# Kernel tuning notes

Hardware: AMD Instinct MI355X
Metric: run time of the kernel (lower is better)

The kernel has to match this reference:

```python
import jax, jax.numpy as jnp
import numpy as np

A = 9  # len(scales) * len(ratios) anchor templates
DN = ('NHWC', 'HWIO', 'NHWC')


def _conv(x, w, b):
    y = jax.lax.conv_general_dilated(x, w, window_strides=(1, 1), padding='SAME',
                                     dimension_numbers=DN)
    return y + b


def setup_inputs() -> dict:
    key = jax.random.key(0)
    ks = jax.random.split(key, 9)
    s = 0.02  # weight init scale
    x = jax.random.normal(ks[0], (4, 128, 128, 512), jnp.float32)
    W1 = jax.random.normal(ks[1], (3, 3, 512, 256), jnp.float32) * s
    b1 = jnp.zeros((256,), jnp.float32)
    W2 = jax.random.normal(ks[2], (3, 3, 256, 256), jnp.float32) * s
    b2 = jnp.zeros((256,), jnp.float32)
    Wr = jax.random.normal(ks[3], (1, 1, 256, 4 * A), jnp.float32) * s
    br = jnp.zeros((4 * A,), jnp.float32)
    Wc = jax.random.normal(ks[4], (1, 1, 256, 2 * A), jnp.float32) * s
    bc = jnp.zeros((2 * A,), jnp.float32)
    return {'x': x, 'W1': W1, 'b1': b1, 'W2': W2, 'b2': b2,
            'Wr': Wr, 'br': br, 'Wc': Wc, 'bc': bc}


def reference(x, W1, b1, W2, b2, Wr, br, Wc, bc):
    h = jax.nn.relu(_conv(x, W1, b1))
    h = jax.nn.relu(_conv(h, W2, b2))
    B, H, W = h.shape[0], h.shape[1], h.shape[2]
    reg = _conv(h, Wr, br).reshape(B, H, W, A, 4)            # (B,H,W,A,4)
    cls = _conv(h, Wc, bc).reshape(B, H, W, A, 2)            # (B,H,W,A,2)
    cls = jax.nn.softmax(cls, axis=4)
    return jnp.concatenate((cls, reg), axis=4)               # (B,H,W,A,6)
```

## Files before the change

### kernel.cpp

```cpp
#include <hip/hip_runtime.h>


typedef float f32x4  __attribute__((ext_vector_type(4)));
typedef float f32x16 __attribute__((ext_vector_type(16)));
typedef short bf16x8 __attribute__((ext_vector_type(8)));

union U16x8 { uint4 v; unsigned short s[8]; };

__device__ __forceinline__ unsigned short f2bf(float f) {
  union { float f; unsigned int u; } v; v.f = f;
  unsigned int r = v.u + 0x7FFFu + ((v.u >> 16) & 1u);
  return (unsigned short)(r >> 16);
}

#define GLOAD_LDS16(G, L)                                        \
  __builtin_amdgcn_global_load_lds(                              \
      (const __attribute__((address_space(1))) void*)(G),        \
      (__attribute__((address_space(3))) void*)(L), 16, 0, 0)

__global__ __launch_bounds__(256) void transpose_cvt(
    const float* __restrict__ src, unsigned short* __restrict__ dst,
    int K, int N) {
  __shared__ float t[32][33];
  const int tx = threadIdx.x, ty = threadIdx.y;
  const int k0 = blockIdx.x * 32, n0 = blockIdx.y * 32;
  const float* s = src + (size_t)blockIdx.z * K * N;
  unsigned short* d = dst + (size_t)blockIdx.z * N * K;
#pragma unroll
  for (int r = 0; r < 32; r += 8) {
    int k = k0 + ty + r, n = n0 + tx;
    t[ty + r][tx] = (k < K && n < N) ? s[(size_t)k * N + n] : 0.f;
  }
  __syncthreads();
#pragma unroll
  for (int r = 0; r < 32; r += 8) {
    int n = n0 + ty + r, k = k0 + tx;
    if (n < N && k < K) d[(size_t)n * K + k] = f2bf(t[tx][ty + r]);
  }
}

__global__ __launch_bounds__(256) void convert_x(
    const float* __restrict__ x, unsigned short* __restrict__ xp) {
  int idx = blockIdx.x * 256 + threadIdx.x;
  int g = idx & 63;
  int cell = idx >> 6;
  int xpix = cell % 130;
  int t = cell / 130;
  int ypix = t % 130;
  int b = t / 130;
  U16x8 u;
  if (xpix == 0 || xpix == 129 || ypix == 0 || ypix == 129) {
    u.v = make_uint4(0u, 0u, 0u, 0u);
  } else {
    const float* sp = x + ((size_t)((b * 128 + ypix - 1) * 128) + (xpix - 1)) * 512 + g * 8;
    float4 a = *(const float4*)sp;
    float4 c = *(const float4*)(sp + 4);
    u.s[0] = f2bf(a.x); u.s[1] = f2bf(a.y); u.s[2] = f2bf(a.z); u.s[3] = f2bf(a.w);
    u.s[4] = f2bf(c.x); u.s[5] = f2bf(c.y); u.s[6] = f2bf(c.z); u.s[7] = f2bf(c.w);
  }
  *(uint4*)(xp + (size_t)cell * 512 + g * 8) = u.v;
}

__global__ __launch_bounds__(256) void zero_h1_borders(unsigned short* __restrict__ h1p) {
  int idx = blockIdx.x * 256 + threadIdx.x;
  int g = idx & 31;
  int cell = idx >> 5;
  int xpix = cell % 130;
  int t = cell / 130;
  int ypix = t % 130;
  if (xpix == 0 || xpix == 129 || ypix == 0 || ypix == 129)
    *(uint4*)(h1p + (size_t)cell * 256 + g * 8) = make_uint4(0u, 0u, 0u, 0u);
}

template<int CIN, int MODE>
__global__ __launch_bounds__(512, 2) void conv3x3(
    const unsigned short* __restrict__ Ap,
    const unsigned short* __restrict__ WT,
    const float* __restrict__ bias,
    unsigned short* __restrict__ out) {
  constexpr int NCI    = CIN / 32;
  constexpr int LOGNCI = (NCI == 16) ? 4 : 3;
  constexpr int NT     = 3 * NCI;
  constexpr int A_BYTES = 8 * 192 * 16;
  constexpr int B_BYTES = 12 * 256 * 16;
  constexpr int BUF     = A_BYTES + B_BYTES;
  __shared__ __align__(16) unsigned char smem[2 * BUF];

  const int tid  = threadIdx.x;
  const int wave = tid >> 6, lane = tid & 63;
  const int l31 = lane & 31, hi = lane >> 5;
  const int wm = wave >> 2, wn = wave & 3;
  const int b = blockIdx.x >> 6;
  const int y0 = (blockIdx.x & 63) * 2;
  const int brow = b * 130 + y0;

  int a_go[3], a_ld[3];
#pragma unroll
  for (int i = 0; i < 3; ++i) {
    int c = (wave * 3 + i) * 64 + lane;
    int px = c % 192, t = c / 192;
    int q = t & 3, rw = t >> 2;
    a_go[i] = (rw * 130 + px) * CIN + q * 8;
    a_ld[i] = (wave * 3 + i) * 1024;
  }
  int b_go[6], b_ld[6];
#pragma unroll
  for (int i = 0; i < 6; ++i) {
    int c = (wave * 6 + i) * 64 + lane;
    int co = c & 255, t = c >> 8;
    int q = t & 3, dxs = t >> 2;
    b_go[i] = (dxs * 256 + co) * CIN + q * 8;
    b_ld[i] = A_BYTES + (wave * 6 + i) * 1024;
  }

  const float bb0 = bias[wn * 64 + l31];
  const float bb1 = bias[wn * 64 + 32 + l31];

  f32x16 acc[4][2] = {};

  auto stage = [&](int tile) {
    const int dy  = tile >> LOGNCI;
    const int ci0 = (tile & (NCI - 1)) << 5;
    unsigned char* sb = smem + (size_t)(tile & 1) * BUF;
    const unsigned short* Ab = Ap + (size_t)(brow + dy) * 130 * CIN + ci0;
#pragma unroll
    for (int i = 0; i < 3; ++i)
      GLOAD_LDS16(Ab + a_go[i], sb + a_ld[i]);
    const unsigned short* Bb = WT + (size_t)dy * 3 * 256 * CIN + ci0;
#pragma unroll
    for (int i = 0; i < 6; ++i)
      GLOAD_LDS16(Bb + b_go[i], sb + b_ld[i]);
  };

  stage(0);
  asm volatile("s_waitcnt vmcnt(0)" ::: "memory");
  __builtin_amdgcn_s_barrier();

#pragma unroll 2
  for (int t = 0; t < NT; ++t) {
    const unsigned char* sb = smem + (size_t)(t & 1) * BUF;
#pragma unroll
    for (int dx = 0; dx < 3; ++dx) {
      bf16x8 af[2][4], bfr[2][2];
#pragma unroll
      for (int ks = 0; ks < 2; ++ks) {
        const int q_ = ks * 2 + hi;
        const int ab = ((wm * 4 + q_) * 192 + dx + l31) * 16;
        const int bb = A_BYTES + ((dx * 4 + q_) * 256 + wn * 64 + l31) * 16;
#pragma unroll
        for (int i = 0; i < 4; ++i)
          af[ks][i] = *(const bf16x8*)(sb + ab + i * 512);
#pragma unroll
        for (int j = 0; j < 2; ++j)
          bfr[ks][j] = *(const bf16x8*)(sb + bb + j * 512);
      }
      if (dx == 0 && t + 1 < NT) stage(t + 1);
      if (dx == 2 && t + 1 < NT)
        asm volatile("s_waitcnt vmcnt(0)" ::: "memory");
      __builtin_amdgcn_sched_barrier(0);
      __builtin_amdgcn_s_barrier();
      asm volatile("s_waitcnt lgkmcnt(0)" ::: "memory");
      __builtin_amdgcn_sched_barrier(0);
      __builtin_amdgcn_s_setprio(1);
#pragma unroll
      for (int ks = 0; ks < 2; ++ks)
#pragma unroll
        for (int i = 0; i < 4; ++i)
#pragma unroll
          for (int j = 0; j < 2; ++j)
            acc[i][j] = __builtin_amdgcn_mfma_f32_32x32x16_bf16(
                af[ks][i], bfr[ks][j], acc[i][j], 0, 0, 0);
      __builtin_amdgcn_s_setprio(0);
      __builtin_amdgcn_sched_barrier(0);
      __builtin_amdgcn_s_barrier();
    }
  }

#pragma unroll
  for (int i = 0; i < 4; ++i) {
#pragma unroll
    for (int j = 0; j < 2; ++j) {
      const int n = wn * 64 + j * 32 + l31;
      const float bb = j ? bb1 : bb0;
#pragma unroll
      for (int reg = 0; reg < 16; ++reg) {
        int px = i * 32 + (reg & 3) + 8 * (reg >> 2) + 4 * hi;
        float v = fmaxf(acc[i][j][reg] + bb, 0.f);
        size_t off;
        if (MODE == 0)
          off = ((size_t)(brow + wm + 1) * 130 + (px + 1)) * 256 + n;
        else
          off = ((size_t)((b * 128 + y0 + wm) * 128) + px) * 256 + n;
        out[off] = f2bf(v);
      }
    }
  }
}

__global__ __launch_bounds__(256) void heads_kernel(
    const unsigned short* __restrict__ h2,
    const unsigned short* __restrict__ WhT,
    const float* __restrict__ br, const float* __restrict__ bc,
    float* __restrict__ out) {
  __shared__ __align__(16) unsigned short As[64][264];
  const int tid = threadIdx.x;
  const int wave = tid >> 6, lane = tid & 63;
  const int quad = lane >> 4, l16 = lane & 15;
  const int pix0 = blockIdx.x * 64;
#pragma unroll
  for (int r = 0; r < 8; ++r) {
    int s = r * 256 + tid;
    int row = s >> 5, seg = s & 31;
    *(uint4*)&As[row][seg * 8] =
        *(const uint4*)(h2 + (size_t)(pix0 + row) * 256 + seg * 8);
  }
  __syncthreads();
  f32x4 acc[4] = {};
#pragma unroll
  for (int ks = 0; ks < 8; ++ks) {
    bf16x8 af = *(const bf16x8*)&As[wave * 16 + l16][ks * 32 + quad * 8];
#pragma unroll
    for (int j = 0; j < 4; ++j) {
      bf16x8 bfr = *(const bf16x8*)(WhT + (size_t)(j * 16 + l16) * 256 + ks * 32 + quad * 8);
      acc[j] = __builtin_amdgcn_mfma_f32_16x16x32_bf16(af, bfr, acc[j], 0, 0, 0);
    }
  }
#pragma unroll
  for (int j = 0; j < 4; ++j) {
    int n = j * 16 + l16;
    float bias = 0.f;
    if (n < 18) bias = bc[n];
    else if (n < 54) bias = br[n - 18];
#pragma unroll
    for (int r = 0; r < 4; ++r) {
      int p = pix0 + wave * 16 + quad * 4 + r;
      float v = acc[j][r] + bias;
      float partner = __shfl_xor(v, 1);
      if (n < 18) {
        float mx = fmaxf(v, partner);
        float e0 = __expf(v - mx), e1 = __expf(partner - mx);
        int a = n >> 1, sl = n & 1;
        out[(size_t)p * 54 + a * 6 + sl] = e0 / (e0 + e1);
      } else if (n < 54) {
        int rr = n - 18, a = rr >> 2, sl = (rr & 3) + 2;
        out[(size_t)p * 54 + a * 6 + sl] = v;
      }
    }
  }
}

extern "C" void kernel_launch(void* const* d_in, const int* in_sizes, int n_in,
                              void* d_out, int out_size, void* d_ws, size_t ws_size,
                              hipStream_t stream) {
  const float* x  = (const float*)d_in[0];
  const float* W1 = (const float*)d_in[1];
  const float* b1 = (const float*)d_in[2];
  const float* W2 = (const float*)d_in[3];
  const float* b2 = (const float*)d_in[4];
  const float* Wr = (const float*)d_in[5];
  const float* br = (const float*)d_in[6];
  const float* Wc = (const float*)d_in[7];
  const float* bc = (const float*)d_in[8];
  float* out = (float*)d_out;

  constexpr size_t XPAD_B  = 4ull * 130 * 130 * 512 * 2;
  constexpr size_t H1PAD_B = 4ull * 130 * 130 * 256 * 2;
  constexpr size_t H2_B    = 4ull * 128 * 128 * 256 * 2;
  constexpr size_t W1T_B   = 9ull * 256 * 512 * 2;
  constexpr size_t W2T_B   = 9ull * 256 * 256 * 2;
  char* ws = (char*)d_ws;
  unsigned short* x_pad  = (unsigned short*)(ws);
  unsigned short* h1_pad = (unsigned short*)(ws + XPAD_B);
  unsigned short* h2     = (unsigned short*)(ws + XPAD_B + H1PAD_B);
  unsigned short* W1T    = (unsigned short*)(ws + XPAD_B + H1PAD_B + H2_B);
  unsigned short* W2T    = (unsigned short*)(ws + XPAD_B + H1PAD_B + H2_B + W1T_B);
  unsigned short* WhT    = (unsigned short*)(ws + XPAD_B + H1PAD_B + H2_B + W1T_B + W2T_B);

  hipMemsetAsync(WhT, 0, 64ull * 256 * 2, stream);
  transpose_cvt<<<dim3(16, 8, 9), dim3(32, 8), 0, stream>>>(W1, W1T, 512, 256);
  transpose_cvt<<<dim3(8, 8, 9),  dim3(32, 8), 0, stream>>>(W2, W2T, 256, 256);
  transpose_cvt<<<dim3(8, 1, 1),  dim3(32, 8), 0, stream>>>(Wc, WhT, 256, 18);
  transpose_cvt<<<dim3(8, 2, 1),  dim3(32, 8), 0, stream>>>(Wr, WhT + 18 * 256, 256, 36);
  convert_x<<<16900, 256, 0, stream>>>(x, x_pad);
  zero_h1_borders<<<8450, 256, 0, stream>>>(h1_pad);
  conv3x3<512, 0><<<256, 512, 0, stream>>>(x_pad, W1T, b1, h1_pad);
  conv3x3<256, 1><<<256, 512, 0, stream>>>(h1_pad, W2T, b2, h2);
  heads_kernel<<<1024, 256, 0, stream>>>(h2, WhT, br, bc, out);
}
```

Measured before the change: 551.9 us.

## Store activations channel-group-major and pre-pack weights per tile for contiguous LDS loads

```diff
diff --git a/kernel.cpp b/kernel.cpp
--- a/kernel.cpp
+++ b/kernel.cpp
@@ -37,6 +37,26 @@
     int n = n0 + ty + r, k = k0 + tx;
     if (n < N && k < K) d[(size_t)n * K + k] = f2bf(t[tx][ty + r]);
   }
+}
+
+__global__ __launch_bounds__(256) void pack_w(
+    const float* __restrict__ W, unsigned short* __restrict__ out, int CIN) {
+  const int NCI = CIN / 32;
+  int tid = blockIdx.x * 256 + threadIdx.x;
+  int co = tid & 255;
+  int q  = (tid >> 8) & 3;
+  int t  = tid >> 10;
+  int dx = t % 3;
+  int r  = t / 3;
+  int kt = r % NCI;
+  int dy = r / NCI;
+  U16x8 u;
+#pragma unroll
+  for (int e = 0; e < 8; ++e) {
+    int ci = kt * 32 + q * 8 + e;
+    u.s[e] = f2bf(W[((size_t)(dy * 3 + dx) * CIN + ci) * 256 + co]);
+  }
+  *(uint4*)(out + (size_t)tid * 8) = u.v;
 }
 
 __global__ __launch_bounds__(256) void convert_x(
@@ -58,30 +78,34 @@
     u.s[0] = f2bf(a.x); u.s[1] = f2bf(a.y); u.s[2] = f2bf(a.z); u.s[3] = f2bf(a.w);
     u.s[4] = f2bf(c.x); u.s[5] = f2bf(c.y); u.s[6] = f2bf(c.z); u.s[7] = f2bf(c.w);
   }
-  *(uint4*)(xp + (size_t)cell * 512 + g * 8) = u.v;
+  *(uint4*)(xp + (((size_t)(b * 130 + ypix) * 64 + g) * 130 + xpix) * 8) = u.v;
 }
 
 __global__ __launch_bounds__(256) void zero_h1_borders(unsigned short* __restrict__ h1p) {
   int idx = blockIdx.x * 256 + threadIdx.x;
-  int g = idx & 31;
-  int cell = idx >> 5;
-  int xpix = cell % 130;
-  int t = cell / 130;
-  int ypix = t % 130;
-  if (xpix == 0 || xpix == 129 || ypix == 0 || ypix == 129)
-    *(uint4*)(h1p + (size_t)cell * 256 + g * 8) = make_uint4(0u, 0u, 0u, 0u);
+  int px = idx % 130;
+  int t = idx / 130;
+  int g = t & 31;
+  int tt = t >> 5;
+  int y = tt % 130;
+  int b = tt / 130;
+  if (px == 0 || px == 129 || y == 0 || y == 129)
+    *(uint4*)(h1p + (((size_t)(b * 130 + y) * 32 + g) * 130 + px) * 8) =
+        make_uint4(0u, 0u, 0u, 0u);
 }
 
 template<int CIN, int MODE>
 __global__ __launch_bounds__(512, 2) void conv3x3(
     const unsigned short* __restrict__ Ap,
-    const unsigned short* __restrict__ WT,
+    const unsigned short* __restrict__ WTp,
     const float* __restrict__ bias,
     unsigned short* __restrict__ out) {
   constexpr int NCI    = CIN / 32;
   constexpr int LOGNCI = (NCI == 16) ? 4 : 3;
   constexpr int NT     = 3 * NCI;
-  constexpr int A_BYTES = 8 * 192 * 16;
+  constexpr int GPR    = CIN / 8;
+  constexpr int PXS    = 136;
+  constexpr int A_BYTES = 8 * PXS * 16;
   constexpr int B_BYTES = 12 * 256 * 16;
   constexpr int BUF     = A_BYTES + B_BYTES;
   __shared__ __align__(16) unsigned char smem[2 * BUF];
@@ -94,23 +118,17 @@
   const int y0 = (blockIdx.x & 63) * 2;
   const int brow = b * 130 + y0;
 
-  int a_go[3], a_ld[3];
+  int a_rel[3], a_c[3];
 #pragma unroll
   for (int i = 0; i < 3; ++i) {
-    int c = (wave * 3 + i) * 64 + lane;
-    int px = c % 192, t = c / 192;
-    int q = t & 3, rw = t >> 2;
-    a_go[i] = (rw * 130 + px) * CIN + q * 8;
-    a_ld[i] = (wave * 3 + i) * 1024;
-  }
-  int b_go[6], b_ld[6];
-#pragma unroll
-  for (int i = 0; i < 6; ++i) {
-    int c = (wave * 6 + i) * 64 + lane;
-    int co = c & 255, t = c >> 8;
-    int q = t & 3, dxs = t >> 2;
-    b_go[i] = (dxs * 256 + co) * CIN + q * 8;
-    b_ld[i] = A_BYTES + (wave * 6 + i) * 1024;
+    int s = wave + i * 8;
+    if (s < 17) {
+      int c = s * 64 + lane;
+      int px = c % PXS, t2 = c / PXS;
+      int q = t2 & 3, rw = t2 >> 2;
+      a_rel[i] = (rw * GPR + q) * 1040 + px * 8;
+      a_c[i] = c * 16;
+    } else { a_rel[i] = 0; a_c[i] = 0; }
   }
 
   const float bb0 = bias[wn * 64 + l31];
@@ -119,17 +137,19 @@
   f32x16 acc[4][2] = {};
 
   auto stage = [&](int tile) {
-    const int dy  = tile >> LOGNCI;
-    const int ci0 = (tile & (NCI - 1)) << 5;
+    const int dy = tile >> LOGNCI;
+    const int kt = tile & (NCI - 1);
     unsigned char* sb = smem + (size_t)(tile & 1) * BUF;
-    const unsigned short* Ab = Ap + (size_t)(brow + dy) * 130 * CIN + ci0;
-#pragma unroll
-    for (int i = 0; i < 3; ++i)
-      GLOAD_LDS16(Ab + a_go[i], sb + a_ld[i]);
-    const unsigned short* Bb = WT + (size_t)dy * 3 * 256 * CIN + ci0;
-#pragma unroll
-    for (int i = 0; i < 6; ++i)
-      GLOAD_LDS16(Bb + b_go[i], sb + b_ld[i]);
+    const unsigned short* Ab = Ap + ((size_t)(brow + dy) * GPR + kt * 4) * 1040;
+    GLOAD_LDS16(Ab + a_rel[0], sb + a_c[0]);
+    GLOAD_LDS16(Ab + a_rel[1], sb + a_c[1]);
+    if (wave == 0) GLOAD_LDS16(Ab + a_rel[2], sb + a_c[2]);
+    const unsigned short* Bb = WTp + (size_t)(dy * NCI + kt) * 24576;
+#pragma unroll
+    for (int i = 0; i < 6; ++i) {
+      int c = (wave * 6 + i) * 64 + lane;
+      GLOAD_LDS16(Bb + (size_t)c * 8, sb + A_BYTES + c * 16);
+    }
   };
 
   stage(0);
@@ -145,7 +165,7 @@
 #pragma unroll
       for (int ks = 0; ks < 2; ++ks) {
         const int q_ = ks * 2 + hi;
-        const int ab = ((wm * 4 + q_) * 192 + dx + l31) * 16;
+        const int ab = ((wm * 4 + q_) * PXS + dx + l31) * 16;
         const int bb = A_BYTES + ((dx * 4 + q_) * 256 + wn * 64 + l31) * 16;
 #pragma unroll
         for (int i = 0; i < 4; ++i)
@@ -188,7 +208,7 @@
         float v = fmaxf(acc[i][j][reg] + bb, 0.f);
         size_t off;
         if (MODE == 0)
-          off = ((size_t)(brow + wm + 1) * 130 + (px + 1)) * 256 + n;
+          off = (((size_t)(brow + wm + 1) * 32 + (n >> 3)) * 130 + (px + 1)) * 8 + (n & 7);
         else
           off = ((size_t)((b * 128 + y0 + wm) * 128) + px) * 256 + n;
         out[off] = f2bf(v);
@@ -277,8 +297,8 @@
   unsigned short* WhT    = (unsigned short*)(ws + XPAD_B + H1PAD_B + H2_B + W1T_B + W2T_B);
 
   hipMemsetAsync(WhT, 0, 64ull * 256 * 2, stream);
-  transpose_cvt<<<dim3(16, 8, 9), dim3(32, 8), 0, stream>>>(W1, W1T, 512, 256);
-  transpose_cvt<<<dim3(8, 8, 9),  dim3(32, 8), 0, stream>>>(W2, W2T, 256, 256);
+  pack_w<<<576, 256, 0, stream>>>(W1, W1T, 512);
+  pack_w<<<288, 256, 0, stream>>>(W2, W2T, 256);
   transpose_cvt<<<dim3(8, 1, 1),  dim3(32, 8), 0, stream>>>(Wc, WhT, 256, 18);
   transpose_cvt<<<dim3(8, 2, 1),  dim3(32, 8), 0, stream>>>(Wr, WhT + 18 * 256, 256, 36);
   convert_x<<<16900, 256, 0, stream>>>(x, x_pad);
```

Result: faster. 462.0 us (-16.3%).
